# Performance work log

Measured on AMD Instinct MI355X. Metric: run time of the kernel, lower is better.

Reference implementation:

```python
import jax, jax.numpy as jnp
import numpy as np

S = 64        # FARGAN_SUBFRAME_SIZE
NSUB = 4      # FARGAN_SUBFRAMES
HOP = 256     # HOPSIZE = NSUB * S
NF = 256      # num_features
GC = 256      # global_channels
IC = NF + GC  # input_channels
B = 64
T = 100

NOISE_KEY = jax.random.key(1)


def _w(k, shape):
    return jax.random.normal(k, shape, dtype=jnp.float32) / np.sqrt(shape[-1]).astype(np.float32)


def setup_inputs() -> dict:
    key = jax.random.key(0)
    ks = jax.random.split(key, 20)
    return {
        'features': jax.random.normal(ks[0], (B, NF, T), dtype=jnp.float32),
        'global_features': jax.random.normal(ks[1], (B, GC, 1), dtype=jnp.float32),
        'in_W1': _w(ks[2], (IC, IC)),
        'in_b1': jnp.zeros((IC,), jnp.float32),
        'in_W2': _w(ks[3], (HOP, IC)),
        'in_b2': jnp.zeros((HOP,), jnp.float32),
        'fw_W': _w(ks[4], (S, 2 * S)),
        'fw_glu_W': _w(ks[5], (S, S)),
        'gru1_Wih': _w(ks[6], (3 * S, 2 * S)),
        'gru1_Whh': _w(ks[7], (3 * S, S)),
        'glu1_W': _w(ks[8], (S, S)),
        'gru2_Wih': _w(ks[9], (3 * S, 2 * S)),
        'gru2_Whh': _w(ks[10], (3 * S, S)),
        'glu2_W': _w(ks[11], (S, S)),
        'gru3_Wih': _w(ks[12], (3 * S, 2 * S)),
        'gru3_Whh': _w(ks[13], (3 * S, S)),
        'glu3_W': _w(ks[14], (S, S)),
        'skip_dense_W': _w(ks[15], (2 * S, 5 * S)),
        'skip_glu_W': _w(ks[16], (2 * S, 2 * S)),
        'out_W': _w(ks[17], (S, 2 * S)),
    }


def _noise(x, k):
    return jnp.clip(x + (jax.random.uniform(k, x.shape, x.dtype) - 0.5) * (1.0 / 127.0), -1.0, 1.0)


def _glu(x, W):
    return x * jax.nn.sigmoid(x @ W.T)


def _gru_cell(x, h, Wih, Whh):
    gi = x @ Wih.T  # [B, 3S]
    gh = h @ Whh.T
    i_r, i_z, i_n = jnp.split(gi, 3, axis=-1)
    h_r, h_z, h_n = jnp.split(gh, 3, axis=-1)
    r = jax.nn.sigmoid(i_r + h_r)
    z = jax.nn.sigmoid(i_z + h_z)
    n = jnp.tanh(i_n + r * h_n)
    return (1.0 - z) * n + z * h


def _forward(features, global_features, in_W1, in_b1, in_W2, in_b2, fw_W, fw_glu_W,
             gru1_Wih, gru1_Whh, glu1_W, gru2_Wih, gru2_Whh, glu2_W,
             gru3_Wih, gru3_Whh, glu3_W, skip_dense_W, skip_glu_W, out_W):
    b = features.shape[0]
    t = features.shape[2]
    g = global_features[:, :, 0]  # [B, GC]

    def subframe_step(sub, prev, st, key):
        h1, h2, h3, s3 = st
        kk = jax.random.split(key, 10)
        sub = _noise(sub, kk[0])
        prev = _noise(prev, kk[1])
        fw = _noise(_glu(jnp.tanh(jnp.concatenate([sub, s3], -1) @ fw_W.T), fw_glu_W), kk[2])
        h1n = _gru_cell(jnp.concatenate([fw, prev], -1), h1, gru1_Wih, gru1_Whh)
        g1 = _noise(_glu(_noise(h1n, kk[3]), glu1_W), kk[4])
        h2n = _gru_cell(jnp.concatenate([g1, prev], -1), h2, gru2_Wih, gru2_Whh)
        g2 = _noise(_glu(_noise(h2n, kk[5]), glu2_W), kk[6])
        h3n = _gru_cell(jnp.concatenate([g2, prev], -1), h3, gru3_Wih, gru3_Whh)
        g3 = _noise(_glu(_noise(h3n, kk[7]), glu3_W), kk[8])
        skip_feats = jnp.concatenate([g1, g2, g3, fw, prev], -1)  # [B, 5S]
        skip = _glu(_noise(jnp.tanh(skip_feats @ skip_dense_W.T), kk[9]), skip_glu_W)
        out = jnp.tanh(skip @ out_W.T)  # [B, S]
        return out, (h1n, h2n, h3n, sub)

    def frame_step(carry, f_t):
        st, prev, i = carry
        x = jnp.tanh(jnp.concatenate([f_t, g], -1) @ in_W1.T + in_b1) @ in_W2.T + in_b2  # [B, HOP]
        outs = []
        for s in range(NSUB):
            k = jax.random.fold_in(NOISE_KEY, i * NSUB + s)
            o, st = subframe_step(x[:, s * S:(s + 1) * S], prev, st, k)
            prev = o
            outs.append(o)
        return (st, prev, i + 1), jnp.concatenate(outs, -1)

    z = jnp.zeros((b, S), features.dtype)
    init = ((z, z, z, z), z, jnp.int32(0))
    xs = jnp.transpose(features, (2, 0, 1))  # [T, B, NF]
    _, ys = jax.lax.scan(frame_step, init, xs)  # [T, B, HOP]
    signal = jnp.transpose(ys, (1, 0, 2)).reshape(b, t * HOP)
    return signal[:, None, :]  # [B, 1, T*HOP]


def reference(features, global_features, in_W1, in_b1, in_W2, in_b2, fw_W, fw_glu_W,
              gru1_Wih, gru1_Whh, glu1_W, gru2_Wih, gru2_Whh, glu2_W,
              gru3_Wih, gru3_Whh, glu3_W, skip_dense_W, skip_glu_W, out_W):
    return _forward(features, global_features, in_W1, in_b1, in_W2, in_b2, fw_W, fw_glu_W,
                    gru1_Wih, gru1_Whh, glu1_W, gru2_Wih, gru2_Whh, glu2_W,
                    gru3_Wih, gru3_Whh, glu3_W, skip_dense_W, skip_glu_W, out_W)
```

## Files before the change

### kernel.cpp

```cpp
#include <hip/hip_runtime.h>
#include <stdint.h>

#define SS 64
#define BB 64
#define TT 100
#define HOPC 256
#define NFC 256
#define GCC 256
#define ICC 512
#define NC (1.0f/127.0f)
#define NBLK 64
#define NTHR 512

#define OFF_FW     0
#define OFF_FWGLU  8192
#define OFF_G1IH   12288
#define OFF_G1HH   36864
#define OFF_GLU1   49152
#define OFF_G2IH   53248
#define OFF_G2HH   77824
#define OFF_GLU2   90112
#define OFF_G3IH   94208
#define OFF_G3HH   118784
#define OFF_GLU3   131072
#define OFF_SKIPD  135168
#define OFF_SKIPG  176128
#define OFF_OUT    192512
#define W_TOTAL    200704
#define XALL_F32   (TT * BB * HOPC)

typedef _Float16 f16;
typedef _Float16 h2 __attribute__((ext_vector_type(2)));
union U16 { uint4 u; h2 h[4]; };

#if __has_builtin(__builtin_amdgcn_fdot2)
#define FDOT2(a, b, c) __builtin_amdgcn_fdot2((a), (b), (c), false)
#else
#define FDOT2(a, b, c) ((c) + (float)(a)[0] * (float)(b)[0] + (float)(a)[1] * (float)(b)[1])
#endif

__device__ __forceinline__ uint32_t rotl32(uint32_t x, int r) {
    return (x << r) | (x >> (32 - r));
}

__device__ __forceinline__ void tf2x32(uint32_t k0, uint32_t k1, uint32_t c0, uint32_t c1,
                                       uint32_t& o0, uint32_t& o1) {
    uint32_t k2 = k0 ^ k1 ^ 0x1BD11BDAu;
    uint32_t x0 = c0 + k0, x1 = c1 + k1;
    x0 += x1; x1 = rotl32(x1, 13); x1 ^= x0;
    x0 += x1; x1 = rotl32(x1, 15); x1 ^= x0;
    x0 += x1; x1 = rotl32(x1, 26); x1 ^= x0;
    x0 += x1; x1 = rotl32(x1, 6);  x1 ^= x0;
    x0 += k1; x1 += k2 + 1u;
    x0 += x1; x1 = rotl32(x1, 17); x1 ^= x0;
    x0 += x1; x1 = rotl32(x1, 29); x1 ^= x0;
    x0 += x1; x1 = rotl32(x1, 16); x1 ^= x0;
    x0 += x1; x1 = rotl32(x1, 24); x1 ^= x0;
    x0 += k2; x1 += k0 + 2u;
    x0 += x1; x1 = rotl32(x1, 13); x1 ^= x0;
    x0 += x1; x1 = rotl32(x1, 15); x1 ^= x0;
    x0 += x1; x1 = rotl32(x1, 26); x1 ^= x0;
    x0 += x1; x1 = rotl32(x1, 6);  x1 ^= x0;
    x0 += k0; x1 += k1 + 3u;
    x0 += x1; x1 = rotl32(x1, 17); x1 ^= x0;
    x0 += x1; x1 = rotl32(x1, 29); x1 ^= x0;
    x0 += x1; x1 = rotl32(x1, 16); x1 ^= x0;
    x0 += x1; x1 = rotl32(x1, 24); x1 ^= x0;
    x0 += k1; x1 += k2 + 4u;
    x0 += x1; x1 = rotl32(x1, 13); x1 ^= x0;
    x0 += x1; x1 = rotl32(x1, 15); x1 ^= x0;
    x0 += x1; x1 = rotl32(x1, 26); x1 ^= x0;
    x0 += x1; x1 = rotl32(x1, 6);  x1 ^= x0;
    x0 += k2; x1 += k0 + 5u;
    o0 = x0; o1 = x1;
}

__device__ __forceinline__ float unifP(uint32_t k0, uint32_t k1, uint32_t m) {
    uint32_t o0, o1;
    tf2x32(k0, k1, 0u, m, o0, o1);
    uint32_t bits = o0 ^ o1;
    return __uint_as_float((bits >> 9) | 0x3f800000u) - 1.0f;
}

__device__ __forceinline__ float clipf(float v) { return fminf(1.0f, fmaxf(-1.0f, v)); }
__device__ __forceinline__ float noiseu(float v, float u) {
    return clipf(v + (u - 0.5f) * NC);
}
__device__ __forceinline__ float sigmf(float v) {
    return __fdividef(1.0f, 1.0f + __expf(-v));
}
__device__ __forceinline__ float tanhfast(float x) {
    float ax = fminf(fabsf(x), 15.0f);
    float e = __expf(2.0f * ax);
    float r = __fdividef(e - 1.0f, e + 1.0f);
    return copysignf(r, x);
}

__device__ __forceinline__ void bar_lds() {
    asm volatile("s_waitcnt lgkmcnt(0)\n\ts_barrier" ::: "memory");
}

__device__ __forceinline__ float red8dpp(float v) {
    int t;
    t = __builtin_amdgcn_update_dpp(0, __float_as_int(v), 0xB1, 0xF, 0xF, true);
    v += __int_as_float(t);
    t = __builtin_amdgcn_update_dpp(0, __float_as_int(v), 0x4E, 0xF, 0xF, true);
    v += __int_as_float(t);
    t = __builtin_amdgcn_update_dpp(0, __float_as_int(v), 0x141, 0xF, 0xF, true);
    v += __int_as_float(t);
    return v;
}

__device__ __forceinline__ float dotU(const U16& w, const U16& x, float acc) {
#pragma unroll
    for (int i = 0; i < 4; ++i) acc = FDOT2(w.h[i], x.h[i], acc);
    return acc;
}

struct WF1  { U16 w[2]; };
struct WGRU { U16 wih[6]; U16 whh[3]; U16 glu; };
struct WSK  { U16 w[10]; };
struct WSG  { U16 w[4]; };

__device__ __forceinline__ void ldF1(const f16* W, int row, int g, WF1& r) {
    const f16* p = W + row * 128 + g * 16;
    r.w[0].u = *(const uint4*)p;
    r.w[1].u = *(const uint4*)(p + 8);
}
__device__ __forceinline__ void ldF2(const f16* W, int row, int g, U16& r) {
    r.u = *(const uint4*)(W + row * 64 + g * 8);
}
__device__ __forceinline__ void ldGRU(const f16* Wih, const f16* Whh, const f16* Glu,
                                      int row, int g, WGRU& r) {
#pragma unroll
    for (int j = 0; j < 3; ++j) {
        const f16* p = Wih + (row + 64 * j) * 128 + g * 16;
        r.wih[2 * j].u     = *(const uint4*)p;
        r.wih[2 * j + 1].u = *(const uint4*)(p + 8);
        r.whh[j].u = *(const uint4*)(Whh + (row + 64 * j) * 64 + g * 8);
    }
    r.glu.u = *(const uint4*)(Glu + row * 64 + g * 8);
}
__device__ __forceinline__ void ldSK(const f16* W, int row, int g, WSK& r) {
#pragma unroll
    for (int j = 0; j < 2; ++j) {
        const f16* p = W + (row + 64 * j) * 320 + g * 40;
#pragma unroll
        for (int i = 0; i < 5; ++i) r.w[5 * j + i].u = *(const uint4*)(p + 8 * i);
    }
}
__device__ __forceinline__ void ldSG(const f16* W, int row, int g, WSG& r) {
#pragma unroll
    for (int j = 0; j < 2; ++j) {
        const f16* p = W + (row + 64 * j) * 128 + g * 16;
        r.w[2 * j].u     = *(const uint4*)p;
        r.w[2 * j + 1].u = *(const uint4*)(p + 8);
    }
}

__device__ __forceinline__ void pinU(U16& r) {
    asm volatile("" : "+v"(r.u.x), "+v"(r.u.y), "+v"(r.u.z), "+v"(r.u.w));
}

struct SrcW { const float* p[14]; };

__global__ __launch_bounds__(256) void fargan_cvtw(SrcW s, f16* __restrict__ dst) {
    const int offs[15] = {0, 8192, 12288, 36864, 49152, 53248, 77824, 90112,
                          94208, 118784, 131072, 135168, 176128, 192512, 200704};
    int i = blockIdx.x * 256 + threadIdx.x;
    if (i >= W_TOTAL) return;
    int sgi = 0;
#pragma unroll
    for (int t = 1; t < 14; ++t) sgi += (i >= offs[t]);
    dst[i] = (f16)s.p[sgi][i - offs[sgi]];
}

__global__ __launch_bounds__(256) void fargan_tr(const float* __restrict__ f,
                                                 float* __restrict__ fT) {
    __shared__ float L[64][104];
    int b = blockIdx.x >> 2, c0 = (blockIdx.x & 3) * 64;
    for (int e = threadIdx.x; e < 6400; e += 256) {
        int r = e / 100, col = e - r * 100;
        L[r][col] = f[b * NFC * TT + (c0 + r) * TT + col];
    }
    __syncthreads();
    for (int e = threadIdx.x; e < 6400; e += 256) {
        int t = e >> 6, c = e & 63;
        fT[(t * BB + b) * NFC + c0 + c] = L[c][t];
    }
}

__global__ __launch_bounds__(256) void fargan_frame(
    const float* __restrict__ fT, const float* __restrict__ gfeat,
    const float* __restrict__ W1, const float* __restrict__ ib1,
    const float* __restrict__ W2, const float* __restrict__ ib2,
    float* __restrict__ xall)
{
    __shared__ __align__(16) float cat[16][ICC];
    __shared__ __align__(16) float zb[16][ICC];
    const int tid = threadIdx.x;
    const int t = blockIdx.x >> 2;
    const int q = blockIdx.x & 3;

    for (int bb = 0; bb < 16; ++bb) {
        int b = q * 16 + bb;
        for (int c = tid; c < ICC; c += 256) {
            float v = (c < NFC) ? fT[(t * BB + b) * NFC + c]
                                : gfeat[b * GCC + (c - NFC)];
            cat[bb][c] = v;
        }
    }
    __syncthreads();

    {
        int rg = tid & 63, bg = tid >> 6;
        int n0 = rg * 8, bb0 = bg * 4;
        float acc[8][4];
#pragma unroll
        for (int r = 0; r < 8; ++r)
#pragma unroll
            for (int j = 0; j < 4; ++j) acc[r][j] = 0.f;
        for (int k = 0; k < ICC; k += 4) {
            float4 cv[4];
#pragma unroll
            for (int j = 0; j < 4; ++j) cv[j] = *(const float4*)&cat[bb0 + j][k];
#pragma unroll
            for (int r = 0; r < 8; ++r) {
                float4 wv = *(const float4*)&W1[(n0 + r) * ICC + k];
#pragma unroll
                for (int j = 0; j < 4; ++j)
                    acc[r][j] += wv.x * cv[j].x + wv.y * cv[j].y + wv.z * cv[j].z + wv.w * cv[j].w;
            }
        }
#pragma unroll
        for (int r = 0; r < 8; ++r) {
            float bias = ib1[n0 + r];
#pragma unroll
            for (int j = 0; j < 4; ++j)
                zb[bb0 + j][n0 + r] = tanhf(acc[r][j] + bias);
        }
    }
    __syncthreads();

    {
        int rg = tid & 63, bg = tid >> 6;
        int n0 = rg * 4, bb0 = bg * 4;
        float acc[4][4];
#pragma unroll
        for (int r = 0; r < 4; ++r)
#pragma unroll
            for (int j = 0; j < 4; ++j) acc[r][j] = 0.f;
        for (int k = 0; k < ICC; k += 4) {
            float4 cv[4];
#pragma unroll
            for (int j = 0; j < 4; ++j) cv[j] = *(const float4*)&zb[bb0 + j][k];
#pragma unroll
            for (int r = 0; r < 4; ++r) {
                float4 wv = *(const float4*)&W2[(n0 + r) * ICC + k];
#pragma unroll
                for (int j = 0; j < 4; ++j)
                    acc[r][j] += wv.x * cv[j].x + wv.y * cv[j].y + wv.z * cv[j].z + wv.w * cv[j].w;
            }
        }
#pragma unroll
        for (int r = 0; r < 4; ++r) {
            float bias = ib2[n0 + r];
#pragma unroll
            for (int j = 0; j < 4; ++j) {
                int b = q * 16 + bb0 + j;
                xall[(t * BB + b) * HOPC + n0 + r] = acc[r][j] + bias;
            }
        }
    }
}

__global__ __launch_bounds__(512) void fargan_seq(
    const float* __restrict__ xall, const f16* __restrict__ wh,
    float* __restrict__ outp)
{
    const int tid = threadIdx.x;
    const int row = tid >> 3;
    const int g = tid & 7;
    const int bg = blockIdx.x;

    __shared__ __align__(16) f16 XH[128];
    __shared__ __align__(16) f16 SKXH[320];
    __shared__ __align__(16) f16 TWH[64], HNH[64];
    __shared__ __align__(16) f16 SPNH[128], SKVH[128];
    __shared__ __align__(16) f16 HH[2][3][64];
    __shared__ __align__(16) float Hf[2][3][64];
    __shared__ __align__(16) float UNF[2][704];
    __shared__ uint32_t KK[401][20];

    WF1 rF1;  ldF1(wh + OFF_FW, row, g, rF1);
    U16 rF2;  ldF2(wh + OFF_FWGLU, row, g, rF2);
    WGRU rG1; ldGRU(wh + OFF_G1IH, wh + OFF_G1HH, wh + OFF_GLU1, row, g, rG1);
    WGRU rG2; ldGRU(wh + OFF_G2IH, wh + OFF_G2HH, wh + OFF_GLU2, row, g, rG2);
    WGRU rG3; ldGRU(wh + OFF_G3IH, wh + OFF_G3HH, wh + OFF_GLU3, row, g, rG3);
    WSG rSG;  ldSG(wh + OFF_SKIPG, row, g, rSG);
    WF1 rOUT; ldF1(wh + OFF_OUT, row, g, rOUT);

    pinU(rF1.w[0]); pinU(rF1.w[1]); pinU(rF2);
#pragma unroll
    for (int j = 0; j < 6; ++j) { pinU(rG1.wih[j]); pinU(rG2.wih[j]); pinU(rG3.wih[j]); }
#pragma unroll
    for (int j = 0; j < 3; ++j) { pinU(rG1.whh[j]); pinU(rG2.whh[j]); pinU(rG3.whh[j]); }
    pinU(rG1.glu); pinU(rG2.glu); pinU(rG3.glu);
#pragma unroll
    for (int j = 0; j < 4; ++j) pinU(rSG.w[j]);
    pinU(rOUT.w[0]); pinU(rOUT.w[1]);

    float prevO = 0.f, xs_old = 0.f;
    if (g == 0) {
#pragma unroll
        for (int i = 0; i < 3; ++i) { Hf[0][i][row] = 0.f; HH[0][i][row] = (f16)0.f; }
        XH[row] = (f16)0.f; XH[64 + row] = (f16)0.f;
    }

    for (int e = tid; e < 4010; e += NTHR) {
        int ii = e / 10, ki = e - ii * 10;
        uint32_t f0, f1; tf2x32(0u, 1u, 0u, (uint32_t)ii, f0, f1);
        uint32_t A, Bv;  tf2x32(f0, f1, 0u, (uint32_t)ki, A, Bv);
        KK[ii][2 * ki] = A; KK[ii][2 * ki + 1] = Bv;
    }
    __syncthreads();

    for (int j = tid; j < 704; j += NTHR) {
        int sl = j >> 6;
        int kx = (sl < 9) ? 2 * sl : 18;
        uint32_t m = (sl < 9) ? (uint32_t)(bg * 64 + (j & 63))
                              : (uint32_t)(bg * 128 + (j - 576));
        UNF[0][j] = unifP(KK[0][kx], KK[0][kx + 1], m);
    }

    float xf0 = xall[(0 * BB + bg) * HOPC + 0 * SS + row];
    float xf1 = xall[(0 * BB + bg) * HOPC + 1 * SS + row];
    float xf2 = xall[(0 * BB + bg) * HOPC + 2 * SS + row];
    float xf3 = xall[(0 * BB + bg) * HOPC + 3 * SS + row];
    __syncthreads();

    for (int t = 0; t < TT; ++t) {
        const int tn = (t + 1 < TT) ? t + 1 : t;
        float xn0 = xall[(tn * BB + bg) * HOPC + 0 * SS + row];
        float xn1 = xall[(tn * BB + bg) * HOPC + 1 * SS + row];
        float xn2 = xall[(tn * BB + bg) * HOPC + 2 * SS + row];
        float xn3 = xall[(tn * BB + bg) * HOPC + 3 * SS + row];

        for (int s = 0; s < 4; ++s) {
            const int idx = t * 4 + s;
            const int p = idx & 1;

            if (g == 0) {
                float u0 = UNF[p][row];
                float u1 = UNF[p][64 + row];
                float xv = (s == 0) ? xf0 : (s == 1) ? xf1 : (s == 2) ? xf2 : xf3;
                float xs = noiseu(xv, u0);
                XH[row] = (f16)xs; XH[64 + row] = (f16)xs_old; xs_old = xs;
                SKXH[256 + row] = (f16)noiseu(prevO, u1);
            }
            bar_lds();

            float twv;
            {
                U16 xa, xb;
                xa.u = *(const uint4*)&XH[g * 16];
                xb.u = *(const uint4*)&XH[g * 16 + 8];
                float a = dotU(rF1.w[0], xa, 0.f);
                a = dotU(rF1.w[1], xb, a);
                twv = tanhfast(red8dpp(a));
                if (g == 0) TWH[row] = (f16)twv;
            }
            bar_lds();

            {
                U16 xa; xa.u = *(const uint4*)&TWH[g * 8];
                if (tid < 256) {
                    int kx = 2 * (tid >> 6);
                    UNF[p ^ 1][tid] = unifP(KK[idx + 1][kx], KK[idx + 1][kx + 1],
                                            (uint32_t)(bg * 64 + (tid & 63)));
                }
                float a = red8dpp(dotU(rF2, xa, 0.f));
                if (g == 0) SKXH[192 + row] = (f16)noiseu(twv * sigmf(a), UNF[p][128 + row]);
            }
            bar_lds();

#define GRU_STEP(RG, XPTR, GI, UH, UG, GOFF, EXTRA)                                         \
            {                                                                               \
                const f16* xin = (XPTR);                                                    \
                U16 xa, xb, xh;                                                             \
                xa.u = *(const uint4*)xin;                                                  \
                xb.u = *(const uint4*)(xin + 8);                                            \
                xh.u = *(const uint4*)&HH[p][GI][g * 8];                                    \
                EXTRA;                                                                      \
                float ai0 = 0, ai1 = 0, ai2 = 0, ah0 = 0, ah1 = 0, ah2 = 0;                 \
                ai0 = dotU(RG.wih[0], xa, ai0); ai0 = dotU(RG.wih[1], xb, ai0);             \
                ai1 = dotU(RG.wih[2], xa, ai1); ai1 = dotU(RG.wih[3], xb, ai1);             \
                ai2 = dotU(RG.wih[4], xa, ai2); ai2 = dotU(RG.wih[5], xb, ai2);             \
                ah0 = dotU(RG.whh[0], xh, ah0);                                             \
                ah1 = dotU(RG.whh[1], xh, ah1);                                             \
                ah2 = dotU(RG.whh[2], xh, ah2);                                             \
                ai0 = red8dpp(ai0); ai1 = red8dpp(ai1); ai2 = red8dpp(ai2);                 \
                ah0 = red8dpp(ah0); ah1 = red8dpp(ah1); ah2 = red8dpp(ah2);                 \
                float hold = Hf[p][GI][row];                                                \
                float r  = sigmf(ai0 + ah0);                                                \
                float z  = sigmf(ai1 + ah1);                                                \
                float nn = tanhfast(ai2 + r * ah2);                                         \
                float hnew = (1.f - z) * nn + z * hold;                                     \
                float hNv = noiseu(hnew, UNF[p][(UH) + row]);                               \
                if (g == 0) {                                                               \
                    Hf[p ^ 1][GI][row] = hnew;                                              \
                    HH[p ^ 1][GI][row] = (f16)hnew;                                         \
                    HNH[row] = (f16)hNv;                                                    \
                }                                                                           \
                bar_lds();                                                                  \
                U16 xg; xg.u = *(const uint4*)&HNH[g * 8];                                  \
                float ag = red8dpp(dotU(RG.glu, xg, 0.f));                                  \
                if (g == 0) SKXH[(GOFF) + row] =                                            \
                    (f16)noiseu(hNv * sigmf(ag), UNF[p][(UG) + row]);                       \
            }                                                                               \
            bar_lds();

#define NOISE_A2 do { if (tid >= 256) {                                                     \
                int kx = 2 * (tid >> 6);                                                    \
                UNF[p ^ 1][tid] = unifP(KK[idx + 1][kx], KK[idx + 1][kx + 1],               \
                                        (uint32_t)(bg * 64 + (tid & 63))); } } while (0)
#define NOISE_B do { int j2 = tid + 512; if (j2 < 704) {                                    \
                int kx = (j2 < 576) ? 16 : 18;                                              \
                uint32_t m2 = (j2 < 576) ? (uint32_t)(bg * 64 + (j2 & 63))                  \
                                         : (uint32_t)(bg * 128 + (j2 - 576));               \
                UNF[p ^ 1][j2] = unifP(KK[idx + 1][kx], KK[idx + 1][kx + 1], m2); } } while (0)

            GRU_STEP(rG1, SKXH + 192 + g * 16, 0, 192, 256, 0, NOISE_A2)
            GRU_STEP(rG2, (g < 4 ? SKXH + g * 16 : SKXH + 256 + (g - 4) * 16), 1, 320, 384, 64, NOISE_B)
            WSK rSK; ldSK(wh + OFF_SKIPD, row, g, rSK);
            GRU_STEP(rG3, (g < 4 ? SKXH + 64 + g * 16 : SKXH + 256 + (g - 4) * 16), 2, 448, 512, 128, ((void)0))
#undef GRU_STEP
#undef NOISE_A2
#undef NOISE_B

            float sp0, sp1;
            {
                U16 xs[5];
#pragma unroll
                for (int i = 0; i < 5; ++i) xs[i].u = *(const uint4*)&SKXH[g * 40 + 8 * i];
                float a0 = 0, a1 = 0;
#pragma unroll
                for (int i = 0; i < 5; ++i) {
                    a0 = dotU(rSK.w[i], xs[i], a0);
                    a1 = dotU(rSK.w[5 + i], xs[i], a1);
                }
                sp0 = noiseu(tanhfast(red8dpp(a0)), UNF[p][576 + row]);
                sp1 = noiseu(tanhfast(red8dpp(a1)), UNF[p][640 + row]);
                if (g == 0) { SPNH[row] = (f16)sp0; SPNH[64 + row] = (f16)sp1; }
            }
            bar_lds();

            {
                U16 xa, xb;
                xa.u = *(const uint4*)&SPNH[g * 16];
                xb.u = *(const uint4*)&SPNH[g * 16 + 8];
                float a0 = dotU(rSG.w[0], xa, 0.f); a0 = dotU(rSG.w[1], xb, a0);
                float a1 = dotU(rSG.w[2], xa, 0.f); a1 = dotU(rSG.w[3], xb, a1);
                a0 = red8dpp(a0); a1 = red8dpp(a1);
                if (g == 0) {
                    SKVH[row]      = (f16)(sp0 * sigmf(a0));
                    SKVH[64 + row] = (f16)(sp1 * sigmf(a1));
                }
            }
            bar_lds();

            {
                U16 xa, xb;
                xa.u = *(const uint4*)&SKVH[g * 16];
                xb.u = *(const uint4*)&SKVH[g * 16 + 8];
                float a = dotU(rOUT.w[0], xa, 0.f);
                a = dotU(rOUT.w[1], xb, a);
                float o = tanhfast(red8dpp(a));
                prevO = o;
                if (g == 0) outp[bg * (TT * HOPC) + t * HOPC + s * SS + row] = o;
            }
        }
        xf0 = xn0; xf1 = xn1; xf2 = xn2; xf3 = xn3;
    }
}

extern "C" void kernel_launch(void* const* d_in, const int* in_sizes, int n_in,
                              void* d_out, int out_size, void* d_ws, size_t ws_size,
                              hipStream_t stream) {
    const float* features = (const float*)d_in[0];
    const float* gfeat    = (const float*)d_in[1];
    const float* W1       = (const float*)d_in[2];
    const float* ib1      = (const float*)d_in[3];
    const float* W2       = (const float*)d_in[4];
    const float* ib2      = (const float*)d_in[5];

    float* xall = (float*)d_ws;
    float* fT   = xall + XALL_F32;
    f16*   wh   = (f16*)(fT + XALL_F32);
    float* outp = (float*)d_out;

    SrcW sw;
    for (int i = 0; i < 14; ++i) sw.p[i] = (const float*)d_in[6 + i];

    hipLaunchKernelGGL(fargan_cvtw, dim3((W_TOTAL + 255) / 256), dim3(256), 0, stream, sw, wh);
    hipLaunchKernelGGL(fargan_tr, dim3(256), dim3(256), 0, stream, features, fT);
    hipLaunchKernelGGL(fargan_frame, dim3(TT * 4), dim3(256), 0, stream,
                       fT, gfeat, W1, ib1, W2, ib2, xall);
    hipLaunchKernelGGL(fargan_seq, dim3(NBLK), dim3(NTHR), 0, stream, xall, wh, outp);
}
```

Before: 2.692 ms.

## Pregenerate all noise uniforms in a parallel kernel before the sequential recurrence

Adds a parallel kernel that computes every per-subframe noise uniform for all batches into workspace, about 72 MB. The sequential kernel then prefetches the next subframe's uniforms from global memory instead of running threefry key derivation and hashing inside its latency-bound loop. This removes the serial RNG work and the large KK shared table, at the cost of a large global buffer and extra memory traffic. The new path is used only when the workspace is big enough; otherwise the old kernel runs.

```diff
diff --git a/kernel.cpp b/kernel.cpp
--- a/kernel.cpp
+++ b/kernel.cpp
@@ -28,6 +28,7 @@
 #define OFF_OUT    192512
 #define W_TOTAL    200704
 #define XALL_F32   (TT * BB * HOPC)
+#define UG_FLOATS  ((size_t)400 * 64 * 704)
 
 typedef _Float16 f16;
 typedef _Float16 h2 __attribute__((ext_vector_type(2)));
@@ -274,9 +275,31 @@
     }
 }
 
-__global__ __launch_bounds__(512) void fargan_seq(
+__global__ __launch_bounds__(256) void fargan_ugen(float* __restrict__ ug) {
+    __shared__ uint32_t kk[20];
+    const int idx = blockIdx.x;
+    const int tid = threadIdx.x;
+    if (tid < 10) {
+        uint32_t f0, f1; tf2x32(0u, 1u, 0u, (uint32_t)idx, f0, f1);
+        uint32_t A, Bv;  tf2x32(f0, f1, 0u, (uint32_t)tid, A, Bv);
+        kk[2 * tid] = A; kk[2 * tid + 1] = Bv;
+    }
+    __syncthreads();
+    float* dst = ug + (size_t)idx * 64 * 704;
+    for (int c = 0; c < 64; ++c) {
+        for (int j = tid; j < 704; j += 256) {
+            int sl = j >> 6;
+            int kx = (sl < 9) ? 2 * sl : 18;
+            uint32_t m = (sl < 9) ? (uint32_t)(c * 64 + (j & 63))
+                                  : (uint32_t)(c * 128 + (j - 576));
+            dst[c * 704 + j] = unifP(kk[kx], kk[kx + 1], m);
+        }
+    }
+}
+
+__global__ __launch_bounds__(512) void fargan_seqpg(
     const float* __restrict__ xall, const f16* __restrict__ wh,
-    float* __restrict__ outp)
+    const float* __restrict__ ug, float* __restrict__ outp)
 {
     const int tid = threadIdx.x;
     const int row = tid >> 3;
@@ -290,7 +313,6 @@
     __shared__ __align__(16) f16 HH[2][3][64];
     __shared__ __align__(16) float Hf[2][3][64];
     __shared__ __align__(16) float UNF[2][704];
-    __shared__ uint32_t KK[401][20];
 
     WF1 rF1;  ldF1(wh + OFF_FW, row, g, rF1);
     U16 rF2;  ldF2(wh + OFF_FWGLU, row, g, rF2);
@@ -317,21 +339,8 @@
         XH[row] = (f16)0.f; XH[64 + row] = (f16)0.f;
     }
 
-    for (int e = tid; e < 4010; e += NTHR) {
-        int ii = e / 10, ki = e - ii * 10;
-        uint32_t f0, f1; tf2x32(0u, 1u, 0u, (uint32_t)ii, f0, f1);
-        uint32_t A, Bv;  tf2x32(f0, f1, 0u, (uint32_t)ki, A, Bv);
-        KK[ii][2 * ki] = A; KK[ii][2 * ki + 1] = Bv;
-    }
-    __syncthreads();
-
-    for (int j = tid; j < 704; j += NTHR) {
-        int sl = j >> 6;
-        int kx = (sl < 9) ? 2 * sl : 18;
-        uint32_t m = (sl < 9) ? (uint32_t)(bg * 64 + (j & 63))
-                              : (uint32_t)(bg * 128 + (j - 576));
-        UNF[0][j] = unifP(KK[0][kx], KK[0][kx + 1], m);
-    }
+    for (int j = tid; j < 704; j += NTHR)
+        UNF[0][j] = ug[(size_t)bg * 704 + j];
 
     float xf0 = xall[(0 * BB + bg) * HOPC + 0 * SS + row];
     float xf1 = xall[(0 * BB + bg) * HOPC + 1 * SS + row];
@@ -349,6 +358,7 @@
         for (int s = 0; s < 4; ++s) {
             const int idx = t * 4 + s;
             const int p = idx & 1;
+            float gl0, gl1;
 
             if (g == 0) {
                 float u0 = UNF[p][row];
@@ -362,6 +372,11 @@
 
             float twv;
             {
+                const int idn = (idx + 1 < 400) ? idx + 1 : 399;
+                const float* gsrc = ug + ((size_t)idn * 64 + bg) * 704;
+                gl0 = gsrc[tid];
+                gl1 = (tid < 192) ? gsrc[512 + tid] : 0.f;
+
                 U16 xa, xb;
                 xa.u = *(const uint4*)&XH[g * 16];
                 xb.u = *(const uint4*)&XH[g * 16 + 8];
@@ -374,17 +389,12 @@
 
             {
                 U16 xa; xa.u = *(const uint4*)&TWH[g * 8];
-                if (tid < 256) {
-                    int kx = 2 * (tid >> 6);
-                    UNF[p ^ 1][tid] = unifP(KK[idx + 1][kx], KK[idx + 1][kx + 1],
-                                            (uint32_t)(bg * 64 + (tid & 63)));
-                }
                 float a = red8dpp(dotU(rF2, xa, 0.f));
                 if (g == 0) SKXH[192 + row] = (f16)noiseu(twv * sigmf(a), UNF[p][128 + row]);
             }
             bar_lds();
 
-#define GRU_STEP(RG, XPTR, GI, UH, UG, GOFF, EXTRA)                                         \
+#define GRU_STEP(RG, XPTR, GI, UH, UG_, GOFF, EXTRA)                                        \
             {                                                                               \
                 const f16* xin = (XPTR);                                                    \
                 U16 xa, xb, xh;                                                             \
@@ -416,27 +426,20 @@
                 U16 xg; xg.u = *(const uint4*)&HNH[g * 8];                                  \
                 float ag = red8dpp(dotU(RG.glu, xg, 0.f));                                  \
                 if (g == 0) SKXH[(GOFF) + row] =                                            \
-                    (f16)noiseu(hNv * sigmf(ag), UNF[p][(UG) + row]);                       \
+                    (f16)noiseu(hNv * sigmf(ag), UNF[p][(UG_) + row]);                      \
             }                                                                               \
             bar_lds();
 
-#define NOISE_A2 do { if (tid >= 256) {                                                     \
-                int kx = 2 * (tid >> 6);                                                    \
-                UNF[p ^ 1][tid] = unifP(KK[idx + 1][kx], KK[idx + 1][kx + 1],               \
-                                        (uint32_t)(bg * 64 + (tid & 63))); } } while (0)
-#define NOISE_B do { int j2 = tid + 512; if (j2 < 704) {                                    \
-                int kx = (j2 < 576) ? 16 : 18;                                              \
-                uint32_t m2 = (j2 < 576) ? (uint32_t)(bg * 64 + (j2 & 63))                  \
-                                         : (uint32_t)(bg * 128 + (j2 - 576));               \
-                UNF[p ^ 1][j2] = unifP(KK[idx + 1][kx], KK[idx + 1][kx + 1], m2); } } while (0)
-
-            GRU_STEP(rG1, SKXH + 192 + g * 16, 0, 192, 256, 0, NOISE_A2)
-            GRU_STEP(rG2, (g < 4 ? SKXH + g * 16 : SKXH + 256 + (g - 4) * 16), 1, 320, 384, 64, NOISE_B)
+#define UNF_STORE do {                                                                      \
+                UNF[p ^ 1][tid] = gl0;                                                      \
+                if (tid < 192) UNF[p ^ 1][512 + tid] = gl1; } while (0)
+
+            GRU_STEP(rG1, SKXH + 192 + g * 16, 0, 192, 256, 0, ((void)0))
+            GRU_STEP(rG2, (g < 4 ? SKXH + g * 16 : SKXH + 256 + (g - 4) * 16), 1, 320, 384, 64, UNF_STORE)
             WSK rSK; ldSK(wh + OFF_SKIPD, row, g, rSK);
             GRU_STEP(rG3, (g < 4 ? SKXH + 64 + g * 16 : SKXH + 256 + (g - 4) * 16), 2, 448, 512, 128, ((void)0))
 #undef GRU_STEP
-#undef NOISE_A2
-#undef NOISE_B
+#undef UNF_STORE
 
             float sp0, sp1;
             {
@@ -484,6 +487,216 @@
     }
 }
 
+__global__ __launch_bounds__(512) void fargan_seq(
+    const float* __restrict__ xall, const f16* __restrict__ wh,
+    float* __restrict__ outp)
+{
+    const int tid = threadIdx.x;
+    const int row = tid >> 3;
+    const int g = tid & 7;
+    const int bg = blockIdx.x;
+
+    __shared__ __align__(16) f16 XH[128];
+    __shared__ __align__(16) f16 SKXH[320];
+    __shared__ __align__(16) f16 TWH[64], HNH[64];
+    __shared__ __align__(16) f16 SPNH[128], SKVH[128];
+    __shared__ __align__(16) f16 HH[2][3][64];
+    __shared__ __align__(16) float Hf[2][3][64];
+    __shared__ __align__(16) float UNF[2][704];
+    __shared__ uint32_t KK[401][20];
+
+    WF1 rF1;  ldF1(wh + OFF_FW, row, g, rF1);
+    U16 rF2;  ldF2(wh + OFF_FWGLU, row, g, rF2);
+    WGRU rG1; ldGRU(wh + OFF_G1IH, wh + OFF_G1HH, wh + OFF_GLU1, row, g, rG1);
+    WGRU rG2; ldGRU(wh + OFF_G2IH, wh + OFF_G2HH, wh + OFF_GLU2, row, g, rG2);
+    WGRU rG3; ldGRU(wh + OFF_G3IH, wh + OFF_G3HH, wh + OFF_GLU3, row, g, rG3);
+    WSG rSG;  ldSG(wh + OFF_SKIPG, row, g, rSG);
+    WF1 rOUT; ldF1(wh + OFF_OUT, row, g, rOUT);
+
+    pinU(rF1.w[0]); pinU(rF1.w[1]); pinU(rF2);
+#pragma unroll
+    for (int j = 0; j < 6; ++j) { pinU(rG1.wih[j]); pinU(rG2.wih[j]); pinU(rG3.wih[j]); }
+#pragma unroll
+    for (int j = 0; j < 3; ++j) { pinU(rG1.whh[j]); pinU(rG2.whh[j]); pinU(rG3.whh[j]); }
+    pinU(rG1.glu); pinU(rG2.glu); pinU(rG3.glu);
+#pragma unroll
+    for (int j = 0; j < 4; ++j) pinU(rSG.w[j]);
+    pinU(rOUT.w[0]); pinU(rOUT.w[1]);
+
+    float prevO = 0.f, xs_old = 0.f;
+    if (g == 0) {
+#pragma unroll
+        for (int i = 0; i < 3; ++i) { Hf[0][i][row] = 0.f; HH[0][i][row] = (f16)0.f; }
+        XH[row] = (f16)0.f; XH[64 + row] = (f16)0.f;
+    }
+
+    for (int e = tid; e < 4010; e += NTHR) {
+        int ii = e / 10, ki = e - ii * 10;
+        uint32_t f0, f1; tf2x32(0u, 1u, 0u, (uint32_t)ii, f0, f1);
+        uint32_t A, Bv;  tf2x32(f0, f1, 0u, (uint32_t)ki, A, Bv);
+        KK[ii][2 * ki] = A; KK[ii][2 * ki + 1] = Bv;
+    }
+    __syncthreads();
+
+    for (int j = tid; j < 704; j += NTHR) {
+        int sl = j >> 6;
+        int kx = (sl < 9) ? 2 * sl : 18;
+        uint32_t m = (sl < 9) ? (uint32_t)(bg * 64 + (j & 63))
+                              : (uint32_t)(bg * 128 + (j - 576));
+        UNF[0][j] = unifP(KK[0][kx], KK[0][kx + 1], m);
+    }
+
+    float xf0 = xall[(0 * BB + bg) * HOPC + 0 * SS + row];
+    float xf1 = xall[(0 * BB + bg) * HOPC + 1 * SS + row];
+    float xf2 = xall[(0 * BB + bg) * HOPC + 2 * SS + row];
+    float xf3 = xall[(0 * BB + bg) * HOPC + 3 * SS + row];
+    __syncthreads();
+
+    for (int t = 0; t < TT; ++t) {
+        const int tn = (t + 1 < TT) ? t + 1 : t;
+        float xn0 = xall[(tn * BB + bg) * HOPC + 0 * SS + row];
+        float xn1 = xall[(tn * BB + bg) * HOPC + 1 * SS + row];
+        float xn2 = xall[(tn * BB + bg) * HOPC + 2 * SS + row];
+        float xn3 = xall[(tn * BB + bg) * HOPC + 3 * SS + row];
+
+        for (int s = 0; s < 4; ++s) {
+            const int idx = t * 4 + s;
+            const int p = idx & 1;
+
+            if (g == 0) {
+                float u0 = UNF[p][row];
+                float u1 = UNF[p][64 + row];
+                float xv = (s == 0) ? xf0 : (s == 1) ? xf1 : (s == 2) ? xf2 : xf3;
+                float xs = noiseu(xv, u0);
+                XH[row] = (f16)xs; XH[64 + row] = (f16)xs_old; xs_old = xs;
+                SKXH[256 + row] = (f16)noiseu(prevO, u1);
+            }
+            bar_lds();
+
+            float twv;
+            {
+                U16 xa, xb;
+                xa.u = *(const uint4*)&XH[g * 16];
+                xb.u = *(const uint4*)&XH[g * 16 + 8];
+                float a = dotU(rF1.w[0], xa, 0.f);
+                a = dotU(rF1.w[1], xb, a);
+                twv = tanhfast(red8dpp(a));
+                if (g == 0) TWH[row] = (f16)twv;
+            }
+            bar_lds();
+
+            {
+                U16 xa; xa.u = *(const uint4*)&TWH[g * 8];
+                if (tid < 256) {
+                    int kx = 2 * (tid >> 6);
+                    UNF[p ^ 1][tid] = unifP(KK[idx + 1][kx], KK[idx + 1][kx + 1],
+                                            (uint32_t)(bg * 64 + (tid & 63)));
+                }
+                float a = red8dpp(dotU(rF2, xa, 0.f));
+                if (g == 0) SKXH[192 + row] = (f16)noiseu(twv * sigmf(a), UNF[p][128 + row]);
+            }
+            bar_lds();
+
+#define GRU_STEP(RG, XPTR, GI, UH, UG_, GOFF, EXTRA)                                        \
+            {                                                                               \
+                const f16* xin = (XPTR);                                                    \
+                U16 xa, xb, xh;                                                             \
+                xa.u = *(const uint4*)xin;                                                  \
+                xb.u = *(const uint4*)(xin + 8);                                            \
+                xh.u = *(const uint4*)&HH[p][GI][g * 8];                                    \
+                EXTRA;                                                                      \
+                float ai0 = 0, ai1 = 0, ai2 = 0, ah0 = 0, ah1 = 0, ah2 = 0;                 \
+                ai0 = dotU(RG.wih[0], xa, ai0); ai0 = dotU(RG.wih[1], xb, ai0);             \
+                ai1 = dotU(RG.wih[2], xa, ai1); ai1 = dotU(RG.wih[3], xb, ai1);             \
+                ai2 = dotU(RG.wih[4], xa, ai2); ai2 = dotU(RG.wih[5], xb, ai2);             \
+                ah0 = dotU(RG.whh[0], xh, ah0);                                             \
+                ah1 = dotU(RG.whh[1], xh, ah1);                                             \
+                ah2 = dotU(RG.whh[2], xh, ah2);                                             \
+                ai0 = red8dpp(ai0); ai1 = red8dpp(ai1); ai2 = red8dpp(ai2);                 \
+                ah0 = red8dpp(ah0); ah1 = red8dpp(ah1); ah2 = red8dpp(ah2);                 \
+                float hold = Hf[p][GI][row];                                                \
+                float r  = sigmf(ai0 + ah0);                                                \
+                float z  = sigmf(ai1 + ah1);                                                \
+                float nn = tanhfast(ai2 + r * ah2);                                         \
+                float hnew = (1.f - z) * nn + z * hold;                                     \
+                float hNv = noiseu(hnew, UNF[p][(UH) + row]);                               \
+                if (g == 0) {                                                               \
+                    Hf[p ^ 1][GI][row] = hnew;                                              \
+                    HH[p ^ 1][GI][row] = (f16)hnew;                                         \
+                    HNH[row] = (f16)hNv;                                                    \
+                }                                                                           \
+                bar_lds();                                                                  \
+                U16 xg; xg.u = *(const uint4*)&HNH[g * 8];                                  \
+                float ag = red8dpp(dotU(RG.glu, xg, 0.f));                                  \
+                if (g == 0) SKXH[(GOFF) + row] =                                            \
+                    (f16)noiseu(hNv * sigmf(ag), UNF[p][(UG_) + row]);                      \
+            }                                                                               \
+            bar_lds();
+
+#define NOISE_A2 do { if (tid >= 256) {                                                     \
+                int kx = 2 * (tid >> 6);                                                    \
+                UNF[p ^ 1][tid] = unifP(KK[idx + 1][kx], KK[idx + 1][kx + 1],               \
+                                        (uint32_t)(bg * 64 + (tid & 63))); } } while (0)
+#define NOISE_B do { int j2 = tid + 512; if (j2 < 704) {                                    \
+                int kx = (j2 < 576) ? 16 : 18;                                              \
+                uint32_t m2 = (j2 < 576) ? (uint32_t)(bg * 64 + (j2 & 63))                  \
+                                         : (uint32_t)(bg * 128 + (j2 - 576));               \
+                UNF[p ^ 1][j2] = unifP(KK[idx + 1][kx], KK[idx + 1][kx + 1], m2); } } while (0)
+
+            GRU_STEP(rG1, SKXH + 192 + g * 16, 0, 192, 256, 0, NOISE_A2)
+            GRU_STEP(rG2, (g < 4 ? SKXH + g * 16 : SKXH + 256 + (g - 4) * 16), 1, 320, 384, 64, NOISE_B)
+            WSK rSK; ldSK(wh + OFF_SKIPD, row, g, rSK);
+            GRU_STEP(rG3, (g < 4 ? SKXH + 64 + g * 16 : SKXH + 256 + (g - 4) * 16), 2, 448, 512, 128, ((void)0))
+#undef GRU_STEP
+#undef NOISE_A2
+#undef NOISE_B
+
+            float sp0, sp1;
+            {
+                U16 xs[5];
+#pragma unroll
+                for (int i = 0; i < 5; ++i) xs[i].u = *(const uint4*)&SKXH[g * 40 + 8 * i];
+                float a0 = 0, a1 = 0;
+#pragma unroll
+                for (int i = 0; i < 5; ++i) {
+                    a0 = dotU(rSK.w[i], xs[i], a0);
+                    a1 = dotU(rSK.w[5 + i], xs[i], a1);
+                }
+                sp0 = noiseu(tanhfast(red8dpp(a0)), UNF[p][576 + row]);
+                sp1 = noiseu(tanhfast(red8dpp(a1)), UNF[p][640 + row]);
+                if (g == 0) { SPNH[row] = (f16)sp0; SPNH[64 + row] = (f16)sp1; }
+            }
+            bar_lds();
+
+            {
+                U16 xa, xb;
+                xa.u = *(const uint4*)&SPNH[g * 16];
+                xb.u = *(const uint4*)&SPNH[g * 16 + 8];
+                float a0 = dotU(rSG.w[0], xa, 0.f); a0 = dotU(rSG.w[1], xb, a0);
+                float a1 = dotU(rSG.w[2], xa, 0.f); a1 = dotU(rSG.w[3], xb, a1);
+                a0 = red8dpp(a0); a1 = red8dpp(a1);
+                if (g == 0) {
+                    SKVH[row]      = (f16)(sp0 * sigmf(a0));
+                    SKVH[64 + row] = (f16)(sp1 * sigmf(a1));
+                }
+            }
+            bar_lds();
+
+            {
+                U16 xa, xb;
+                xa.u = *(const uint4*)&SKVH[g * 16];
+                xb.u = *(const uint4*)&SKVH[g * 16 + 8];
+                float a = dotU(rOUT.w[0], xa, 0.f);
+                a = dotU(rOUT.w[1], xb, a);
+                float o = tanhfast(red8dpp(a));
+                prevO = o;
+                if (g == 0) outp[bg * (TT * HOPC) + t * HOPC + s * SS + row] = o;
+            }
+        }
+        xf0 = xn0; xf1 = xn1; xf2 = xn2; xf3 = xn3;
+    }
+}
+
 extern "C" void kernel_launch(void* const* d_in, const int* in_sizes, int n_in,
                               void* d_out, int out_size, void* d_ws, size_t ws_size,
                               hipStream_t stream) {
@@ -497,7 +710,11 @@
     float* xall = (float*)d_ws;
     float* fT   = xall + XALL_F32;
     f16*   wh   = (f16*)(fT + XALL_F32);
+    float* ug   = (float*)(wh + W_TOTAL);
     float* outp = (float*)d_out;
+
+    const size_t need = (size_t)13508608 + UG_FLOATS * 4;
+    const bool pregen = (ws_size >= need);
 
     SrcW sw;
     for (int i = 0; i < 14; ++i) sw.p[i] = (const float*)d_in[6 + i];
@@ -506,5 +723,11 @@
     hipLaunchKernelGGL(fargan_tr, dim3(256), dim3(256), 0, stream, features, fT);
     hipLaunchKernelGGL(fargan_frame, dim3(TT * 4), dim3(256), 0, stream,
                        fT, gfeat, W1, ib1, W2, ib2, xall);
-    hipLaunchKernelGGL(fargan_seq, dim3(NBLK), dim3(NTHR), 0, stream, xall, wh, outp);
-}
+    if (pregen) {
+        hipLaunchKernelGGL(fargan_ugen, dim3(400), dim3(256), 0, stream, ug);
+        hipLaunchKernelGGL(fargan_seqpg, dim3(NBLK), dim3(NTHR), 0, stream,
+                           xall, wh, ug, outp);
+    } else {
+        hipLaunchKernelGGL(fargan_seq, dim3(NBLK), dim3(NTHR), 0, stream, xall, wh, outp);
+    }
+}
```

Result: faster. 2.562 ms (-4.8%).

## Rewrite sequential subframe kernel with MFMA and pregenerated noise buffer

Applied to the files above, without the earlier changes.

Adds a new sequential kernel that computes the small matvecs with 16x16x32 f16 MFMA instructions in place of fdot2 plus DPP reductions. Warps are split into GRU-gate and GLU/output roles, and the skip-dense weights are staged in padded LDS. A separate kernel pregenerates all Threefry uniform noise into workspace so the serial loop only loads it. The new path runs only when the workspace is large enough; otherwise the old kernel is used. Each MFMA is used as a matrix-vector product with a single useful column, and the pregenerated buffer adds roughly 72 MB of global traffic.

```diff
diff --git a/kernel.cpp b/kernel.cpp
--- a/kernel.cpp
+++ b/kernel.cpp
@@ -11,6 +11,7 @@
 #define NC (1.0f/127.0f)
 #define NBLK 64
 #define NTHR 512
+#define SKW_STRIDE 328
 
 #define OFF_FW     0
 #define OFF_FWGLU  8192
@@ -28,9 +29,13 @@
 #define OFF_OUT    192512
 #define W_TOTAL    200704
 #define XALL_F32   (TT * BB * HOPC)
+#define UG_FLOATS  ((size_t)400 * 64 * 704)
 
 typedef _Float16 f16;
 typedef _Float16 h2 __attribute__((ext_vector_type(2)));
+typedef _Float16 f16x4v __attribute__((ext_vector_type(4)));
+typedef _Float16 f16x8v __attribute__((ext_vector_type(8)));
+typedef float f32x4v __attribute__((ext_vector_type(4)));
 union U16 { uint4 u; h2 h[4]; };
 
 #if __has_builtin(__builtin_amdgcn_fdot2)
@@ -38,6 +43,8 @@
 #else
 #define FDOT2(a, b, c) ((c) + (float)(a)[0] * (float)(b)[0] + (float)(a)[1] * (float)(b)[1])
 #endif
+
+#define MFMA16(a, b, c) __builtin_amdgcn_mfma_f32_16x16x32_f16((a), (b), (c), 0, 0, 0)
 
 __device__ __forceinline__ uint32_t rotl32(uint32_t x, int r) {
     return (x << r) | (x >> (32 - r));
@@ -117,6 +124,18 @@
     return acc;
 }
 
+__device__ __forceinline__ f16x8v ldfragG(const f16* W, int K, int rowbase, int kc, int l) {
+    return *(const f16x8v*)(W + (size_t)(rowbase + (l & 15)) * K + kc * 32 + ((l >> 4) << 3));
+}
+__device__ __forceinline__ f16x8v ldbL(const f16* base, int l) {
+    return *(const f16x8v*)(base + ((l >> 4) << 3));
+}
+__device__ __forceinline__ float sel4(f32x4v v, int r) {
+    float a = (r & 1) ? v[1] : v[0];
+    float b = (r & 1) ? v[3] : v[2];
+    return (r & 2) ? b : a;
+}
+
 struct WF1  { U16 w[2]; };
 struct WGRU { U16 wih[6]; U16 whh[3]; U16 glu; };
 struct WSK  { U16 w[10]; };
@@ -157,7 +176,6 @@
         r.w[2 * j + 1].u = *(const uint4*)(p + 8);
     }
 }
-
 __device__ __forceinline__ void pinU(U16& r) {
     asm volatile("" : "+v"(r.u.x), "+v"(r.u.y), "+v"(r.u.z), "+v"(r.u.w));
 }
@@ -274,6 +292,272 @@
     }
 }
 
+__global__ __launch_bounds__(256) void fargan_ugen(float* __restrict__ ug) {
+    __shared__ uint32_t kk[20];
+    const int idx = blockIdx.x;
+    const int tid = threadIdx.x;
+    if (tid < 10) {
+        uint32_t f0, f1; tf2x32(0u, 1u, 0u, (uint32_t)idx, f0, f1);
+        uint32_t A, Bv;  tf2x32(f0, f1, 0u, (uint32_t)tid, A, Bv);
+        kk[2 * tid] = A; kk[2 * tid + 1] = Bv;
+    }
+    __syncthreads();
+    float* dst = ug + (size_t)idx * 64 * 704;
+    for (int c = 0; c < 64; ++c) {
+        for (int j = tid; j < 704; j += 256) {
+            int sl = j >> 6;
+            int kx = (sl < 9) ? 2 * sl : 18;
+            uint32_t m = (sl < 9) ? (uint32_t)(c * 64 + (j & 63))
+                                  : (uint32_t)(c * 128 + (j - 576));
+            dst[c * 704 + j] = unifP(kk[kx], kk[kx + 1], m);
+        }
+    }
+}
+
+__global__ __launch_bounds__(512) void fargan_seqmf(
+    const float* __restrict__ xall, const f16* __restrict__ wh,
+    const float* __restrict__ ug, float* __restrict__ outp)
+{
+    const int tid = threadIdx.x;
+    const int w = tid >> 6;
+    const int l = tid & 63;
+    const int bg = blockIdx.x;
+    const int rsel = l & 3;
+    const int subg = (l >> 4) << 2;
+
+    __shared__ __align__(16) f16 XH[128];
+    __shared__ __align__(16) f16 SKXH[320];
+    __shared__ __align__(16) f16 TWH[64];
+    __shared__ __align__(16) f16 HNH[64];
+    __shared__ __align__(16) float HNF[64];
+    __shared__ __align__(16) f16 SPNH[128];
+    __shared__ __align__(16) float SPN[128];
+    __shared__ __align__(16) f16 SKVH[128];
+    __shared__ __align__(16) f16 HH[2][3][64];
+    __shared__ __align__(16) float Hf[2][3][64];
+    __shared__ __align__(16) float UNF[2][704];
+    __shared__ __align__(16) float XSO[64];
+    extern __shared__ __align__(16) f16 SKW[];
+
+    const f32x4v z4 = {0.f, 0.f, 0.f, 0.f};
+
+    f16x8v aiW[3][3][4], ahW[3][3][2];
+    f16x8v f1W[4], f2W[2], glW[3][2], outW[4];
+    f16x8v sgW[4];
+    if (w < 4) {
+        const int q = w;
+        const int GIH[3] = {OFF_G1IH, OFF_G2IH, OFF_G3IH};
+        const int GHH[3] = {OFF_G1HH, OFF_G2HH, OFF_G3HH};
+#pragma unroll
+        for (int GI = 0; GI < 3; ++GI)
+#pragma unroll
+            for (int gt = 0; gt < 3; ++gt) {
+#pragma unroll
+                for (int kc = 0; kc < 4; ++kc)
+                    aiW[GI][gt][kc] = ldfragG(wh + GIH[GI], 128, gt * 64 + q * 16, kc, l);
+#pragma unroll
+                for (int kc = 0; kc < 2; ++kc)
+                    ahW[GI][gt][kc] = ldfragG(wh + GHH[GI], 64, gt * 64 + q * 16, kc, l);
+            }
+    } else {
+        const int u = w - 4;
+        const int GLU[3] = {OFF_GLU1, OFF_GLU2, OFF_GLU3};
+#pragma unroll
+        for (int kc = 0; kc < 4; ++kc) f1W[kc] = ldfragG(wh + OFF_FW, 128, u * 16, kc, l);
+#pragma unroll
+        for (int kc = 0; kc < 2; ++kc) f2W[kc] = ldfragG(wh + OFF_FWGLU, 64, u * 16, kc, l);
+#pragma unroll
+        for (int GI = 0; GI < 3; ++GI)
+#pragma unroll
+            for (int kc = 0; kc < 2; ++kc)
+                glW[GI][kc] = ldfragG(wh + GLU[GI], 64, u * 16, kc, l);
+#pragma unroll
+        for (int kc = 0; kc < 4; ++kc) outW[kc] = ldfragG(wh + OFF_OUT, 128, u * 16, kc, l);
+    }
+#pragma unroll
+    for (int kc = 0; kc < 4; ++kc) sgW[kc] = ldfragG(wh + OFF_SKIPG, 128, w * 16, kc, l);
+
+    for (int e = tid; e < 128 * 40; e += NTHR) {
+        int r = e / 40, c8 = e - r * 40;
+        *(f16x8v*)&SKW[r * SKW_STRIDE + c8 * 8] =
+            *(const f16x8v*)(wh + OFF_SKIPD + r * 320 + c8 * 8);
+    }
+
+    if (tid < 64) {
+        XSO[tid] = 0.f; XH[tid] = (f16)0.f; XH[64 + tid] = (f16)0.f;
+#pragma unroll
+        for (int GI = 0; GI < 3; ++GI) { Hf[0][GI][tid] = 0.f; HH[0][GI][tid] = (f16)0.f; }
+    }
+    for (int j = tid; j < 704; j += NTHR) UNF[0][j] = ug[(size_t)bg * 704 + j];
+    __syncthreads();
+    if (tid < 64) SKXH[256 + tid] = (f16)noiseu(0.f, UNF[0][64 + tid]);
+
+    float xf0 = xall[(0 * BB + bg) * HOPC + 0 * SS + (tid & 63)];
+    float xf1 = xall[(0 * BB + bg) * HOPC + 1 * SS + (tid & 63)];
+    float xf2 = xall[(0 * BB + bg) * HOPC + 2 * SS + (tid & 63)];
+    float xf3 = xall[(0 * BB + bg) * HOPC + 3 * SS + (tid & 63)];
+    __syncthreads();
+
+    for (int t = 0; t < TT; ++t) {
+        const int tn = (t + 1 < TT) ? t + 1 : t;
+        float xn0 = xall[(tn * BB + bg) * HOPC + 0 * SS + (tid & 63)];
+        float xn1 = xall[(tn * BB + bg) * HOPC + 1 * SS + (tid & 63)];
+        float xn2 = xall[(tn * BB + bg) * HOPC + 2 * SS + (tid & 63)];
+        float xn3 = xall[(tn * BB + bg) * HOPC + 3 * SS + (tid & 63)];
+
+        for (int s = 0; s < 4; ++s) {
+            const int idx = t * 4 + s;
+            const int p = idx & 1;
+            float gl0, gl1, twv = 0.f;
+            f32x4v accRZ[3][2], accHN[3];
+            f16x8v skW[10];
+
+            if (tid < 64) {
+                float u0 = UNF[p][tid];
+                float xv = (s == 0) ? xf0 : (s == 1) ? xf1 : (s == 2) ? xf2 : xf3;
+                float xs = noiseu(xv, u0);
+                float old = XSO[tid];
+                XSO[tid] = xs;
+                XH[tid] = (f16)xs; XH[64 + tid] = (f16)old;
+            }
+            bar_lds();
+
+            {
+                const int idn = (idx + 1 < 400) ? idx + 1 : 399;
+                const float* gsrc = ug + ((size_t)idn * 64 + bg) * 704;
+                gl0 = gsrc[tid];
+                gl1 = (tid < 192) ? gsrc[512 + tid] : 0.f;
+            }
+            if (w >= 4) {
+                const int u = w - 4;
+                f32x4v acc = z4;
+#pragma unroll
+                for (int kc = 0; kc < 4; ++kc)
+                    acc = MFMA16(f1W[kc], ldbL(&XH[kc * 32], l), acc);
+                twv = tanhfast(sel4(acc, rsel));
+                if ((l & 12) == 0) TWH[u * 16 + subg + rsel] = (f16)twv;
+            } else {
+#pragma unroll
+                for (int GI = 0; GI < 3; ++GI) {
+                    f16x8v b0 = ldbL(&HH[p][GI][0], l), b1 = ldbL(&HH[p][GI][32], l);
+                    accRZ[GI][0] = MFMA16(ahW[GI][0][1], b1, MFMA16(ahW[GI][0][0], b0, z4));
+                    accRZ[GI][1] = MFMA16(ahW[GI][1][1], b1, MFMA16(ahW[GI][1][0], b0, z4));
+                    accHN[GI]    = MFMA16(ahW[GI][2][1], b1, MFMA16(ahW[GI][2][0], b0, z4));
+                }
+            }
+            bar_lds();
+
+            if (w >= 4) {
+                const int u = w - 4;
+                f32x4v acc = MFMA16(f2W[1], ldbL(&TWH[32], l),
+                                    MFMA16(f2W[0], ldbL(&TWH[0], l), z4));
+                const int ROW = u * 16 + subg + rsel;
+                float fv = noiseu(twv * sigmf(sel4(acc, rsel)), UNF[p][128 + ROW]);
+                if ((l & 12) == 0) SKXH[192 + ROW] = (f16)fv;
+            }
+            bar_lds();
+
+#define GRU_CORE(GI, B0, B1, B2, B3, UH)                                                    \
+            if (w < 4) {                                                                    \
+                f16x8v b0 = ldbL(&SKXH[B0], l), b1 = ldbL(&SKXH[B1], l);                    \
+                f16x8v b2 = ldbL(&SKXH[B2], l), b3 = ldbL(&SKXH[B3], l);                    \
+                f32x4v aR = accRZ[GI][0], aZ = accRZ[GI][1], aN = z4;                       \
+                aR = MFMA16(aiW[GI][0][0], b0, aR); aR = MFMA16(aiW[GI][0][1], b1, aR);     \
+                aR = MFMA16(aiW[GI][0][2], b2, aR); aR = MFMA16(aiW[GI][0][3], b3, aR);     \
+                aZ = MFMA16(aiW[GI][1][0], b0, aZ); aZ = MFMA16(aiW[GI][1][1], b1, aZ);     \
+                aZ = MFMA16(aiW[GI][1][2], b2, aZ); aZ = MFMA16(aiW[GI][1][3], b3, aZ);     \
+                aN = MFMA16(aiW[GI][2][0], b0, aN); aN = MFMA16(aiW[GI][2][1], b1, aN);     \
+                aN = MFMA16(aiW[GI][2][2], b2, aN); aN = MFMA16(aiW[GI][2][3], b3, aN);     \
+                const int ROW = w * 16 + subg + rsel;                                       \
+                float vr = sel4(aR, rsel), vz = sel4(aZ, rsel);                             \
+                float vin = sel4(aN, rsel), vhn = sel4(accHN[GI], rsel);                    \
+                float hold = Hf[p][GI][ROW];                                                \
+                float rr = sigmf(vr), zz = sigmf(vz);                                       \
+                float nn = tanhfast(vin + rr * vhn);                                        \
+                float hnew = (1.f - zz) * nn + zz * hold;                                   \
+                float hNv = noiseu(hnew, UNF[p][(UH) + ROW]);                               \
+                if ((l & 12) == 0) {                                                        \
+                    Hf[p ^ 1][GI][ROW] = hnew;                                              \
+                    HH[p ^ 1][GI][ROW] = (f16)hnew;                                         \
+                    HNH[ROW] = (f16)hNv;                                                    \
+                    HNF[ROW] = hNv;                                                         \
+                }                                                                           \
+            }                                                                               \
+            bar_lds();
+
+#define GLU_SEG(GI, GOFF, UG_, EXTRA)                                                       \
+            EXTRA;                                                                          \
+            if (w >= 4) {                                                                   \
+                const int u = w - 4;                                                        \
+                f32x4v acc = MFMA16(glW[GI][1], ldbL(&HNH[32], l),                          \
+                                    MFMA16(glW[GI][0], ldbL(&HNH[0], l), z4));              \
+                const int ROW = u * 16 + subg + rsel;                                       \
+                float val = noiseu(HNF[ROW] * sigmf(sel4(acc, rsel)),                       \
+                                   UNF[p][(UG_) + ROW]);                                    \
+                if ((l & 12) == 0) SKXH[(GOFF) + ROW] = (f16)val;                           \
+            }                                                                               \
+            bar_lds();
+
+#define S7EXTRA do {                                                                        \
+                UNF[p ^ 1][tid] = gl0;                                                      \
+                if (tid < 192) UNF[p ^ 1][512 + tid] = gl1;                                 \
+                _Pragma("unroll")                                                           \
+                for (int kc = 0; kc < 10; ++kc)                                             \
+                    skW[kc] = *(const f16x8v*)&SKW[(w * 16 + (l & 15)) * SKW_STRIDE         \
+                                                   + kc * 32 + ((l >> 4) << 3)];            \
+            } while (0)
+
+            GRU_CORE(0, 192, 224, 256, 288, 192)
+            GLU_SEG(0, 0, 256, ((void)0))
+            GRU_CORE(1, 0, 32, 256, 288, 320)
+            GLU_SEG(1, 64, 384, S7EXTRA)
+            GRU_CORE(2, 64, 96, 256, 288, 448)
+            GLU_SEG(2, 128, 512, ((void)0))
+#undef GRU_CORE
+#undef GLU_SEG
+#undef S7EXTRA
+
+            {
+                f32x4v acc = z4;
+#pragma unroll
+                for (int kc = 0; kc < 10; ++kc)
+                    acc = MFMA16(skW[kc], ldbL(&SKXH[kc * 32], l), acc);
+                const int ROW = w * 16 + subg + rsel;
+                float sp = noiseu(tanhfast(sel4(acc, rsel)), UNF[p][576 + ROW]);
+                if ((l & 12) == 0) { SPNH[ROW] = (f16)sp; SPN[ROW] = sp; }
+            }
+            bar_lds();
+
+            {
+                f32x4v acc = z4;
+#pragma unroll
+                for (int kc = 0; kc < 4; ++kc)
+                    acc = MFMA16(sgW[kc], ldbL(&SPNH[kc * 32], l), acc);
+                const int ROW = w * 16 + subg + rsel;
+                float sk = SPN[ROW] * sigmf(sel4(acc, rsel));
+                if ((l & 12) == 0) SKVH[ROW] = (f16)sk;
+            }
+            bar_lds();
+
+            if (w >= 4) {
+                const int u = w - 4;
+                f32x4v acc = z4;
+#pragma unroll
+                for (int kc = 0; kc < 4; ++kc)
+                    acc = MFMA16(outW[kc], ldbL(&SKVH[kc * 32], l), acc);
+                const int ROW = u * 16 + subg + rsel;
+                float o = tanhfast(sel4(acc, rsel));
+                float pn = noiseu(o, UNF[p ^ 1][64 + ROW]);
+                if ((l & 12) == 0) {
+                    outp[bg * (TT * HOPC) + t * HOPC + s * SS + ROW] = o;
+                    SKXH[256 + ROW] = (f16)pn;
+                }
+            }
+        }
+        xf0 = xn0; xf1 = xn1; xf2 = xn2; xf3 = xn3;
+    }
+}
+
 __global__ __launch_bounds__(512) void fargan_seq(
     const float* __restrict__ xall, const f16* __restrict__ wh,
     float* __restrict__ outp)
@@ -384,7 +668,7 @@
             }
             bar_lds();
 
-#define GRU_STEP(RG, XPTR, GI, UH, UG, GOFF, EXTRA)                                         \
+#define GRU_STEP(RG, XPTR, GI, UH, UG_, GOFF, EXTRA)                                        \
             {                                                                               \
                 const f16* xin = (XPTR);                                                    \
                 U16 xa, xb, xh;                                                             \
@@ -416,7 +700,7 @@
                 U16 xg; xg.u = *(const uint4*)&HNH[g * 8];                                  \
                 float ag = red8dpp(dotU(RG.glu, xg, 0.f));                                  \
                 if (g == 0) SKXH[(GOFF) + row] =                                            \
-                    (f16)noiseu(hNv * sigmf(ag), UNF[p][(UG) + row]);                       \
+                    (f16)noiseu(hNv * sigmf(ag), UNF[p][(UG_) + row]);                      \
             }                                                                               \
             bar_lds();
 
@@ -497,7 +781,11 @@
     float* xall = (float*)d_ws;
     float* fT   = xall + XALL_F32;
     f16*   wh   = (f16*)(fT + XALL_F32);
+    float* ug   = (float*)(wh + W_TOTAL);
     float* outp = (float*)d_out;
+
+    const size_t need = (size_t)13508608 + UG_FLOATS * 4;
+    const bool pregen = (ws_size >= need);
 
     SrcW sw;
     for (int i = 0; i < 14; ++i) sw.p[i] = (const float*)d_in[6 + i];
@@ -506,5 +794,12 @@
     hipLaunchKernelGGL(fargan_tr, dim3(256), dim3(256), 0, stream, features, fT);
     hipLaunchKernelGGL(fargan_frame, dim3(TT * 4), dim3(256), 0, stream,
                        fT, gfeat, W1, ib1, W2, ib2, xall);
-    hipLaunchKernelGGL(fargan_seq, dim3(NBLK), dim3(NTHR), 0, stream, xall, wh, outp);
-}
+    if (pregen) {
+        hipLaunchKernelGGL(fargan_ugen, dim3(400), dim3(256), 0, stream, ug);
+        hipLaunchKernelGGL(fargan_seqmf, dim3(NBLK), dim3(NTHR),
+                           128 * SKW_STRIDE * sizeof(f16), stream,
+                           xall, wh, ug, outp);
+    } else {
+        hipLaunchKernelGGL(fargan_seq, dim3(NBLK), dim3(NTHR), 0, stream, xall, wh, outp);
+    }
+}
```

After: 4.142 ms. 53.9% more time.
